# Optimization experiments

Measured on AMD Instinct MI355X. Metric: run time of the kernel, lower is better.

Reference implementation:

```python
import jax, jax.numpy as jnp
import numpy as np

B, T, D_MODEL, N_HEAD = 2, 2048, 1024, 16
HEAD_DIM = D_MODEL // N_HEAD


def setup_inputs() -> dict:
    key = jax.random.key(0)
    ks = jax.random.split(key, 4)
    s = 0.02
    return {
        "x": jax.random.normal(ks[0], (B, T, D_MODEL), dtype=jnp.float32),
        "freqs_cis": jnp.zeros((T, HEAD_DIM // 2), dtype=jnp.float32),  # unused under ALiBi
        "Wq": jax.random.normal(ks[1], (D_MODEL, D_MODEL), dtype=jnp.float32) * s,
        "bq": jnp.zeros((D_MODEL,), dtype=jnp.float32),
        "Wkv": jax.random.normal(ks[2], (2 * D_MODEL, D_MODEL), dtype=jnp.float32) * s,
        "bkv": jnp.zeros((2 * D_MODEL,), dtype=jnp.float32),
        "Wo": jax.random.normal(ks[3], (D_MODEL, D_MODEL), dtype=jnp.float32) * s,
        "bo": jnp.zeros((D_MODEL,), dtype=jnp.float32),
    }


def reference(x, freqs_cis, Wq, bq, Wkv, bkv, Wo, bo):
    Bb, Tt, C = x.shape
    H, Dh = N_HEAD, HEAD_DIM
    # projections (torch Linear: x @ W^T + b)
    q = (x @ Wq.T + bq).reshape(Bb, Tt, H, Dh).transpose(0, 2, 1, 3)      # [B,H,T,Dh]
    kv = (x @ Wkv.T + bkv).reshape(Bb, Tt, 2, H, Dh).transpose(2, 0, 3, 1, 4)
    k, v = kv[0], kv[1]                                                    # [B,H,T,Dh]
    scores = jnp.einsum('bhqd,bhkd->bhqk', q, k) * (1.0 / np.sqrt(Dh))
    # ALiBi: linear slopes (1/H ... 1.0), bias = slope * (j - i)
    slopes = jnp.arange(1, H + 1, dtype=jnp.float32) / H                   # [H]
    pos = jnp.arange(Tt, dtype=jnp.float32)
    dist = pos[None, :] - pos[:, None]                                     # [T,T], j - i
    scores = scores + slopes[:, None, None] * dist[None]                   # broadcast over B
    # causal mask (upper triangle -> -inf)
    causal = pos[:, None] >= pos[None, :]                                  # [T,T] keep-mask
    scores = jnp.where(causal[None, None], scores, -jnp.inf)
    attn = jax.nn.softmax(scores, axis=-1)
    y = jnp.einsum('bhqk,bhkd->bhqd', attn, v)                             # [B,H,T,Dh]
    y = y.transpose(0, 2, 1, 3).reshape(Bb, Tt, C)
    return y @ Wo.T + bo
```

## Files before the change

kernel.cpp:

```cpp
#include <hip/hip_runtime.h>

typedef unsigned short u16;
typedef __bf16 bf16x8 __attribute__((ext_vector_type(8)));
typedef unsigned short u16x8 __attribute__((ext_vector_type(8)));
typedef float f32x4 __attribute__((ext_vector_type(4)));

#define GP 72
#define KEY(r) ((((r) ^ ((r) >> 3)) & 7) << 3)
#define VKEY(d) ((((d) >> 3) & 7) << 3)

static __device__ __forceinline__ u16 f2b(float f) {
  union { float f; unsigned u; } x; x.f = f;
  unsigned r = x.u + 0x7FFFu + ((x.u >> 16) & 1u);
  return (u16)(r >> 16);
}

static __device__ __forceinline__ bf16x8 ld_frag(const u16* p) {
  union { u16x8 s; bf16x8 b; } u;
  u.s = *reinterpret_cast<const u16x8*>(p);
  return u.b;
}

__global__ __launch_bounds__(256) void cvt_f32_bf16(const float* __restrict__ in,
                                                    u16* __restrict__ out, int n4) {
  int i = blockIdx.x * 256 + threadIdx.x;
  if (i >= n4) return;
  float4 v = reinterpret_cast<const float4*>(in)[i];
  ushort4 o;
  o.x = f2b(v.x); o.y = f2b(v.y); o.z = f2b(v.z); o.w = f2b(v.w);
  reinterpret_cast<ushort4*>(out)[i] = o;
}

__global__ __launch_bounds__(256) void gemm_bt2(
    const u16* __restrict__ A, const u16* __restrict__ Bt,
    const float* __restrict__ bias, void* __restrict__ outp,
    int M, int N, int K, float scale, int out_bf16) {
  __shared__ alignas(16) u16 As[128 * 64];
  __shared__ alignas(16) u16 Bs[64 * 64];
  const int tid = threadIdx.x, wid = tid >> 6, lane = tid & 63;
  const int wr = wid >> 1, wc = wid & 1;
  const int row0 = blockIdx.x * 128, col0 = blockIdx.y * 64;
  const int lr = lane >> 3;
  const int lc = (lane & 7) * 8;
  const int frow = lane & 15, fk = (lane >> 4) * 8;
  f32x4 acc[4][2] = {};

  for (int k0 = 0; k0 < K; k0 += 64) {
    __syncthreads();
#pragma unroll
    for (int t = 0; t < 4; ++t) {
      const int r = wid * 32 + t * 8 + lr;
      __builtin_amdgcn_global_load_lds(
          (const __attribute__((address_space(1))) unsigned int*)(
              A + (size_t)(row0 + r) * K + k0 + (lc ^ KEY(r))),
          (__attribute__((address_space(3))) unsigned int*)(As + (wid * 32 + t * 8) * 64),
          16, 0, 0);
    }
#pragma unroll
    for (int t = 0; t < 2; ++t) {
      const int r = wid * 16 + t * 8 + lr;
      __builtin_amdgcn_global_load_lds(
          (const __attribute__((address_space(1))) unsigned int*)(
              Bt + (size_t)(col0 + r) * K + k0 + (lc ^ KEY(r))),
          (__attribute__((address_space(3))) unsigned int*)(Bs + (wid * 16 + t * 8) * 64),
          16, 0, 0);
    }
    __syncthreads();
#pragma unroll
    for (int ks = 0; ks < 2; ++ks) {
      bf16x8 a[4], b[2];
#pragma unroll
      for (int m = 0; m < 4; ++m) {
        const int r = wr * 64 + m * 16 + frow;
        a[m] = ld_frag(&As[r * 64 + ((ks * 32 + fk) ^ KEY(r))]);
      }
#pragma unroll
      for (int n = 0; n < 2; ++n) {
        const int r = wc * 32 + n * 16 + frow;
        b[n] = ld_frag(&Bs[r * 64 + ((ks * 32 + fk) ^ KEY(r))]);
      }
#pragma unroll
      for (int m = 0; m < 4; ++m)
#pragma unroll
        for (int n = 0; n < 2; ++n)
          acc[m][n] = __builtin_amdgcn_mfma_f32_16x16x32_bf16(a[m], b[n], acc[m][n], 0, 0, 0);
    }
  }
  const int colL = lane & 15, rb = (lane >> 4) * 4;
#pragma unroll
  for (int n = 0; n < 2; ++n) {
    const int gc = col0 + wc * 32 + n * 16 + colL;
    const float bv = bias[gc];
#pragma unroll
    for (int m = 0; m < 4; ++m)
#pragma unroll
      for (int r = 0; r < 4; ++r) {
        const int gr = row0 + wr * 64 + m * 16 + rb + r;
        const float v = (acc[m][n][r] + bv) * scale;
        if (out_bf16) reinterpret_cast<u16*>(outp)[(size_t)gr * N + gc] = f2b(v);
        else reinterpret_cast<float*>(outp)[(size_t)gr * N + gc] = v;
      }
  }
}

__global__ __launch_bounds__(256) void attn_kernel(
    const u16* __restrict__ qb,
    const u16* __restrict__ kvb,
    u16* __restrict__ yb,
    int T) {
  const int C = 1024;
  const int bh = blockIdx.x;
  const int qt = gridDim.y - 1 - blockIdx.y;
  const int b = bh >> 4, h = bh & 15;
  const float slope = (float)(h + 1) * 0.0625f;
  const int tid = threadIdx.x, wid = tid >> 6, lane = tid & 63;
  const int qBase = qt * 64;

  __shared__ alignas(16) u16 Ks[64 * GP];
  __shared__ alignas(16) u16 Vt[64 * GP];
  __shared__ alignas(16) u16 Ps[4][16 * GP];

  const int frow = lane & 15, fk = (lane >> 4) * 8;
  const int col = lane & 15, rb = (lane >> 4) * 4;

  const int q_row = qBase + wid * 16 + frow;
  const u16* qp = qb + (size_t)(b * T + q_row) * C + h * 64;
  const bf16x8 aq0 = ld_frag(qp + fk);
  const bf16x8 aq1 = ld_frag(qp + 32 + fk);

  float mrow[4] = {-1e30f, -1e30f, -1e30f, -1e30f};
  float lrow[4] = {0.f, 0.f, 0.f, 0.f};
  f32x4 accO[4] = {};

  const int sr = tid >> 3;
  const int sc = (tid & 7) * 8;

  for (int kt = 0; kt <= qt; ++kt) {
    const int kBase = kt * 64;
    __syncthreads();
    {
      const size_t g0 = (size_t)(b * T + kBase + sr) * 2048 + h * 64 + sc;
      const size_t g1 = (size_t)(b * T + kBase + sr + 32) * 2048 + h * 64 + sc;
      *reinterpret_cast<int4*>(&Ks[sr * GP + sc]) = *reinterpret_cast<const int4*>(&kvb[g0]);
      *reinterpret_cast<int4*>(&Ks[(sr + 32) * GP + sc]) = *reinterpret_cast<const int4*>(&kvb[g1]);
      int4 v0 = *reinterpret_cast<const int4*>(&kvb[g0 + 1024]);
      int4 v1 = *reinterpret_cast<const int4*>(&kvb[g1 + 1024]);
      const u16* p0 = reinterpret_cast<const u16*>(&v0);
      const u16* p1 = reinterpret_cast<const u16*>(&v1);
      const int kx = VKEY(sc);
#pragma unroll
      for (int j = 0; j < 8; ++j) {
        const int d = sc + j;
        Vt[d * GP + (sr ^ kx)] = p0[j];
        Vt[d * GP + ((sr + 32) ^ kx)] = p1[j];
      }
    }
    __syncthreads();

    f32x4 accS[4] = {};
#pragma unroll
    for (int n = 0; n < 4; ++n) {
      bf16x8 bk0 = ld_frag(&Ks[(n * 16 + frow) * GP + fk]);
      accS[n] = __builtin_amdgcn_mfma_f32_16x16x32_bf16(aq0, bk0, accS[n], 0, 0, 0);
      bf16x8 bk1 = ld_frag(&Ks[(n * 16 + frow) * GP + 32 + fk]);
      accS[n] = __builtin_amdgcn_mfma_f32_16x16x32_bf16(aq1, bk1, accS[n], 0, 0, 0);
    }

#pragma unroll
    for (int r = 0; r < 4; ++r) {
      const int qg = qBase + wid * 16 + rb + r;
      float s[4];
      float tmax = -1e30f;
#pragma unroll
      for (int n = 0; n < 4; ++n) {
        const int kg = kBase + n * 16 + col;
        float v = accS[n][r] + slope * (float)(kg - qg);
        if (kg > qg) v = -1e30f;
        s[n] = v;
        tmax = fmaxf(tmax, v);
      }
      tmax = fmaxf(tmax, __shfl_xor(tmax, 1));
      tmax = fmaxf(tmax, __shfl_xor(tmax, 2));
      tmax = fmaxf(tmax, __shfl_xor(tmax, 4));
      tmax = fmaxf(tmax, __shfl_xor(tmax, 8));
      const float newm = fmaxf(mrow[r], tmax);
      const float corr = __expf(mrow[r] - newm);
      mrow[r] = newm;
      float psum = 0.f;
#pragma unroll
      for (int n = 0; n < 4; ++n) {
        const float p = __expf(s[n] - newm);
        psum += p;
        Ps[wid][(rb + r) * GP + n * 16 + col] = f2b(p);
      }
      psum += __shfl_xor(psum, 1);
      psum += __shfl_xor(psum, 2);
      psum += __shfl_xor(psum, 4);
      psum += __shfl_xor(psum, 8);
      lrow[r] = lrow[r] * corr + psum;
#pragma unroll
      for (int n = 0; n < 4; ++n) accO[n][r] *= corr;
    }

#pragma unroll
    for (int ks = 0; ks < 2; ++ks) {
      bf16x8 ap = ld_frag(&Ps[wid][frow * GP + ks * 32 + fk]);
#pragma unroll
      for (int n = 0; n < 4; ++n) {
        const int d = n * 16 + frow;
        bf16x8 bv = ld_frag(&Vt[d * GP + ((ks * 32 + fk) ^ VKEY(d))]);
        accO[n] = __builtin_amdgcn_mfma_f32_16x16x32_bf16(ap, bv, accO[n], 0, 0, 0);
      }
    }
  }

#pragma unroll
  for (int r = 0; r < 4; ++r) {
    const float inv = 1.0f / lrow[r];
    const int qg = qBase + wid * 16 + rb + r;
    u16* yrow = yb + (size_t)(b * T + qg) * C + h * 64;
#pragma unroll
    for (int n = 0; n < 4; ++n) yrow[n * 16 + col] = f2b(accO[n][r] * inv);
  }
}

extern "C" void kernel_launch(void* const* d_in, const int* in_sizes, int n_in,
                              void* d_out, int out_size, void* d_ws, size_t ws_size,
                              hipStream_t stream) {
  const float* x   = (const float*)d_in[0];
  const float* Wq  = (const float*)d_in[2];
  const float* bq  = (const float*)d_in[3];
  const float* Wkv = (const float*)d_in[4];
  const float* bkv = (const float*)d_in[5];
  const float* Wo  = (const float*)d_in[6];
  const float* bo  = (const float*)d_in[7];
  float* out = (float*)d_out;

  const int B = 2, T = 2048, C = 1024;
  const int M = B * T;

  char* ws = (char*)d_ws;
  u16* xb   = (u16*)(ws + 0);
  u16* wqb  = (u16*)(ws + 8388608);
  u16* wkvb = (u16*)(ws + 10485760);
  u16* wob  = (u16*)(ws + 14680064);
  u16* qb   = (u16*)(ws + 16777216);
  u16* kvb  = (u16*)(ws + 25165824);
  u16* yb   = (u16*)(ws + 41943040);

  cvt_f32_bf16<<<(M * C / 4 + 255) / 256, 256, 0, stream>>>(x, xb, M * C / 4);
  cvt_f32_bf16<<<(C * C / 4 + 255) / 256, 256, 0, stream>>>(Wq, wqb, C * C / 4);
  cvt_f32_bf16<<<(2 * C * C / 4 + 255) / 256, 256, 0, stream>>>(Wkv, wkvb, 2 * C * C / 4);
  cvt_f32_bf16<<<(C * C / 4 + 255) / 256, 256, 0, stream>>>(Wo, wob, C * C / 4);

  gemm_bt2<<<dim3(M / 128, C / 64), 256, 0, stream>>>(xb, wqb, bq, qb, M, C, C, 0.125f, 1);
  gemm_bt2<<<dim3(M / 128, 2 * C / 64), 256, 0, stream>>>(xb, wkvb, bkv, kvb, M, 2 * C, C, 1.0f, 1);
  attn_kernel<<<dim3(B * 16, T / 64), 256, 0, stream>>>(qb, kvb, yb, T);
  gemm_bt2<<<dim3(M / 128, C / 64), 256, 0, stream>>>(yb, wob, bo, out, M, C, C, 1.0f, 0);
}
```

Before: 238.2 us.

## Fuse QKV GEMMs, enlarge GEMM tiles, restructure attention with prefetch and swizzle

Merges the Q and KV projection GEMMs into one launch and doubles the GEMM N-tile to 128, giving each block 4x4 MFMA accumulators for more operand reuse. The attention kernel now uses 32-query tiles with 2 waves per block and register-prefetches the next K/V tile while the current one is computed. It also replaces padded LDS rows with XOR swizzles, adds s_setprio around the MFMA sections, and hoists the ALiBi bias out of the row loop. The trade-offs are higher register pressure in the GEMM, fewer waves per attention block, and more attention blocks in total.

```diff
diff --git a/kernel.cpp b/kernel.cpp
--- a/kernel.cpp
+++ b/kernel.cpp
@@ -5,9 +5,7 @@
 typedef unsigned short u16x8 __attribute__((ext_vector_type(8)));
 typedef float f32x4 __attribute__((ext_vector_type(4)));
 
-#define GP 72
 #define KEY(r) ((((r) ^ ((r) >> 3)) & 7) << 3)
-#define VKEY(d) ((((d) >> 3) & 7) << 3)
 
 static __device__ __forceinline__ u16 f2b(float f) {
   union { float f; unsigned u; } x; x.f = f;
@@ -31,19 +29,19 @@
   reinterpret_cast<ushort4*>(out)[i] = o;
 }
 
-__global__ __launch_bounds__(256) void gemm_bt2(
+template <bool OUT_BF16>
+static __device__ __forceinline__ void gemm_body(
     const u16* __restrict__ A, const u16* __restrict__ Bt,
     const float* __restrict__ bias, void* __restrict__ outp,
-    int M, int N, int K, float scale, int out_bf16) {
+    int N, int K, int row0, int col0, float scale) {
   __shared__ alignas(16) u16 As[128 * 64];
-  __shared__ alignas(16) u16 Bs[64 * 64];
+  __shared__ alignas(16) u16 Bs[128 * 64];
   const int tid = threadIdx.x, wid = tid >> 6, lane = tid & 63;
   const int wr = wid >> 1, wc = wid & 1;
-  const int row0 = blockIdx.x * 128, col0 = blockIdx.y * 64;
   const int lr = lane >> 3;
   const int lc = (lane & 7) * 8;
   const int frow = lane & 15, fk = (lane >> 4) * 8;
-  f32x4 acc[4][2] = {};
+  f32x4 acc[4][4] = {};
 
   for (int k0 = 0; k0 < K; k0 += 64) {
     __syncthreads();
@@ -57,39 +55,39 @@
           16, 0, 0);
     }
 #pragma unroll
-    for (int t = 0; t < 2; ++t) {
-      const int r = wid * 16 + t * 8 + lr;
+    for (int t = 0; t < 4; ++t) {
+      const int r = wid * 32 + t * 8 + lr;
       __builtin_amdgcn_global_load_lds(
           (const __attribute__((address_space(1))) unsigned int*)(
               Bt + (size_t)(col0 + r) * K + k0 + (lc ^ KEY(r))),
-          (__attribute__((address_space(3))) unsigned int*)(Bs + (wid * 16 + t * 8) * 64),
+          (__attribute__((address_space(3))) unsigned int*)(Bs + (wid * 32 + t * 8) * 64),
           16, 0, 0);
     }
     __syncthreads();
 #pragma unroll
     for (int ks = 0; ks < 2; ++ks) {
-      bf16x8 a[4], b[2];
+      bf16x8 a[4], b[4];
 #pragma unroll
       for (int m = 0; m < 4; ++m) {
         const int r = wr * 64 + m * 16 + frow;
         a[m] = ld_frag(&As[r * 64 + ((ks * 32 + fk) ^ KEY(r))]);
       }
 #pragma unroll
-      for (int n = 0; n < 2; ++n) {
-        const int r = wc * 32 + n * 16 + frow;
+      for (int n = 0; n < 4; ++n) {
+        const int r = wc * 64 + n * 16 + frow;
         b[n] = ld_frag(&Bs[r * 64 + ((ks * 32 + fk) ^ KEY(r))]);
       }
 #pragma unroll
       for (int m = 0; m < 4; ++m)
 #pragma unroll
-        for (int n = 0; n < 2; ++n)
+        for (int n = 0; n < 4; ++n)
           acc[m][n] = __builtin_amdgcn_mfma_f32_16x16x32_bf16(a[m], b[n], acc[m][n], 0, 0, 0);
     }
   }
   const int colL = lane & 15, rb = (lane >> 4) * 4;
 #pragma unroll
-  for (int n = 0; n < 2; ++n) {
-    const int gc = col0 + wc * 32 + n * 16 + colL;
+  for (int n = 0; n < 4; ++n) {
+    const int gc = col0 + wc * 64 + n * 16 + colL;
     const float bv = bias[gc];
 #pragma unroll
     for (int m = 0; m < 4; ++m)
@@ -97,13 +95,33 @@
       for (int r = 0; r < 4; ++r) {
         const int gr = row0 + wr * 64 + m * 16 + rb + r;
         const float v = (acc[m][n][r] + bv) * scale;
-        if (out_bf16) reinterpret_cast<u16*>(outp)[(size_t)gr * N + gc] = f2b(v);
-        else reinterpret_cast<float*>(outp)[(size_t)gr * N + gc] = v;
-      }
-  }
-}
-
-__global__ __launch_bounds__(256) void attn_kernel(
+        if constexpr (OUT_BF16)
+          reinterpret_cast<u16*>(outp)[(size_t)gr * N + gc] = f2b(v);
+        else
+          reinterpret_cast<float*>(outp)[(size_t)gr * N + gc] = v;
+      }
+  }
+}
+
+__global__ __launch_bounds__(256) void gemm_qkv(
+    const u16* __restrict__ xb, const u16* __restrict__ wqb,
+    const u16* __restrict__ wkvb, const float* __restrict__ bq,
+    const float* __restrict__ bkv, u16* __restrict__ qb, u16* __restrict__ kvb) {
+  const int row0 = blockIdx.x * 128;
+  const int by = blockIdx.y;
+  const u16* Bt; const float* bias; u16* out; int N, col0; float scale;
+  if (by < 8) { Bt = wqb;  bias = bq;  out = qb;  N = 1024; col0 = by * 128;      scale = 0.125f; }
+  else        { Bt = wkvb; bias = bkv; out = kvb; N = 2048; col0 = (by - 8) * 128; scale = 1.0f; }
+  gemm_body<true>(xb, Bt, bias, out, N, 1024, row0, col0, scale);
+}
+
+__global__ __launch_bounds__(256) void gemm_o(
+    const u16* __restrict__ yb, const u16* __restrict__ wob,
+    const float* __restrict__ bo, float* __restrict__ out) {
+  gemm_body<false>(yb, wob, bo, out, 1024, 1024, blockIdx.x * 128, blockIdx.y * 128, 1.0f);
+}
+
+__global__ __launch_bounds__(128) void attn_kernel(
     const u16* __restrict__ qb,
     const u16* __restrict__ kvb,
     u16* __restrict__ yb,
@@ -114,14 +132,15 @@
   const int b = bh >> 4, h = bh & 15;
   const float slope = (float)(h + 1) * 0.0625f;
   const int tid = threadIdx.x, wid = tid >> 6, lane = tid & 63;
-  const int qBase = qt * 64;
-
-  __shared__ alignas(16) u16 Ks[64 * GP];
-  __shared__ alignas(16) u16 Vt[64 * GP];
-  __shared__ alignas(16) u16 Ps[4][16 * GP];
+  const int qBase = qt * 32;
+
+  __shared__ alignas(16) u16 Ks[64 * 64];
+  __shared__ alignas(16) u16 Vt[64 * 64];
+  __shared__ alignas(16) u16 Ps[2][16 * 64];
 
   const int frow = lane & 15, fk = (lane >> 4) * 8;
   const int col = lane & 15, rb = (lane >> 4) * 4;
+  const int pk = ((lane >> 4) & 3) << 3;
 
   const int q_row = qBase + wid * 16 + frow;
   const u16* qp = qb + (size_t)(b * T + q_row) * C + h * 64;
@@ -132,40 +151,60 @@
   float lrow[4] = {0.f, 0.f, 0.f, 0.f};
   f32x4 accO[4] = {};
 
-  const int sr = tid >> 3;
-  const int sc = (tid & 7) * 8;
-
-  for (int kt = 0; kt <= qt; ++kt) {
+  const int st_r = tid >> 3;
+  const int st_c = (tid & 7) * 8;
+  const int vkj = tid & 7;
+
+  const int nt = (qBase + 31) / 64 + 1;
+
+  int4 kreg[4], vreg[4];
+#pragma unroll
+  for (int t = 0; t < 4; ++t) {
+    const int r = st_r + 16 * t;
+    const size_t g = (size_t)(b * T + r) * 2048 + h * 64 + st_c;
+    kreg[t] = *reinterpret_cast<const int4*>(&kvb[g]);
+    vreg[t] = *reinterpret_cast<const int4*>(&kvb[g + 1024]);
+  }
+
+  for (int kt = 0; kt < nt; ++kt) {
     const int kBase = kt * 64;
+#pragma unroll
+    for (int t = 0; t < 4; ++t) {
+      const int r = st_r + 16 * t;
+      *reinterpret_cast<int4*>(&Ks[r * 64 + (st_c ^ KEY(r))]) = kreg[t];
+      const u16* pv = reinterpret_cast<const u16*>(&vreg[t]);
+#pragma unroll
+      for (int j = 0; j < 8; ++j) {
+        const int d = st_c + j;
+        Vt[d * 64 + (r ^ ((((j) ^ vkj) & 7) << 3))] = pv[j];
+      }
+    }
     __syncthreads();
-    {
-      const size_t g0 = (size_t)(b * T + kBase + sr) * 2048 + h * 64 + sc;
-      const size_t g1 = (size_t)(b * T + kBase + sr + 32) * 2048 + h * 64 + sc;
-      *reinterpret_cast<int4*>(&Ks[sr * GP + sc]) = *reinterpret_cast<const int4*>(&kvb[g0]);
-      *reinterpret_cast<int4*>(&Ks[(sr + 32) * GP + sc]) = *reinterpret_cast<const int4*>(&kvb[g1]);
-      int4 v0 = *reinterpret_cast<const int4*>(&kvb[g0 + 1024]);
-      int4 v1 = *reinterpret_cast<const int4*>(&kvb[g1 + 1024]);
-      const u16* p0 = reinterpret_cast<const u16*>(&v0);
-      const u16* p1 = reinterpret_cast<const u16*>(&v1);
-      const int kx = VKEY(sc);
-#pragma unroll
-      for (int j = 0; j < 8; ++j) {
-        const int d = sc + j;
-        Vt[d * GP + (sr ^ kx)] = p0[j];
-        Vt[d * GP + ((sr + 32) ^ kx)] = p1[j];
-      }
-    }
-    __syncthreads();
+    if (kt + 1 < nt) {
+#pragma unroll
+      for (int t = 0; t < 4; ++t) {
+        const int r = st_r + 16 * t;
+        const size_t g = (size_t)(b * T + kBase + 64 + r) * 2048 + h * 64 + st_c;
+        kreg[t] = *reinterpret_cast<const int4*>(&kvb[g]);
+        vreg[t] = *reinterpret_cast<const int4*>(&kvb[g + 1024]);
+      }
+    }
 
     f32x4 accS[4] = {};
+    __builtin_amdgcn_s_setprio(1);
 #pragma unroll
     for (int n = 0; n < 4; ++n) {
-      bf16x8 bk0 = ld_frag(&Ks[(n * 16 + frow) * GP + fk]);
+      const int r = n * 16 + frow;
+      bf16x8 bk0 = ld_frag(&Ks[r * 64 + (fk ^ KEY(r))]);
       accS[n] = __builtin_amdgcn_mfma_f32_16x16x32_bf16(aq0, bk0, accS[n], 0, 0, 0);
-      bf16x8 bk1 = ld_frag(&Ks[(n * 16 + frow) * GP + 32 + fk]);
+      bf16x8 bk1 = ld_frag(&Ks[r * 64 + ((32 + fk) ^ KEY(r))]);
       accS[n] = __builtin_amdgcn_mfma_f32_16x16x32_bf16(aq1, bk1, accS[n], 0, 0, 0);
     }
-
+    __builtin_amdgcn_s_setprio(0);
+
+    float bn[4]; int kg[4];
+#pragma unroll
+    for (int n = 0; n < 4; ++n) { kg[n] = kBase + n * 16 + col; bn[n] = slope * (float)kg[n]; }
 #pragma unroll
     for (int r = 0; r < 4; ++r) {
       const int qg = qBase + wid * 16 + rb + r;
@@ -173,9 +212,8 @@
       float tmax = -1e30f;
 #pragma unroll
       for (int n = 0; n < 4; ++n) {
-        const int kg = kBase + n * 16 + col;
-        float v = accS[n][r] + slope * (float)(kg - qg);
-        if (kg > qg) v = -1e30f;
+        float v = accS[n][r] + bn[n];
+        if (kg[n] > qg) v = -1e30f;
         s[n] = v;
         tmax = fmaxf(tmax, v);
       }
@@ -191,7 +229,7 @@
       for (int n = 0; n < 4; ++n) {
         const float p = __expf(s[n] - newm);
         psum += p;
-        Ps[wid][(rb + r) * GP + n * 16 + col] = f2b(p);
+        Ps[wid][(rb + r) * 64 + ((n * 16 + col) ^ pk)] = f2b(p);
       }
       psum += __shfl_xor(psum, 1);
       psum += __shfl_xor(psum, 2);
@@ -202,16 +240,20 @@
       for (int n = 0; n < 4; ++n) accO[n][r] *= corr;
     }
 
+    __builtin_amdgcn_s_setprio(1);
 #pragma unroll
     for (int ks = 0; ks < 2; ++ks) {
-      bf16x8 ap = ld_frag(&Ps[wid][frow * GP + ks * 32 + fk]);
+      const int pkr = ((frow >> 2) & 3) << 3;
+      bf16x8 ap = ld_frag(&Ps[wid][frow * 64 + ((ks * 32 + fk) ^ pkr)]);
 #pragma unroll
       for (int n = 0; n < 4; ++n) {
         const int d = n * 16 + frow;
-        bf16x8 bv = ld_frag(&Vt[d * GP + ((ks * 32 + fk) ^ VKEY(d))]);
+        bf16x8 bv = ld_frag(&Vt[d * 64 + ((ks * 32 + fk) ^ KEY(d))]);
         accO[n] = __builtin_amdgcn_mfma_f32_16x16x32_bf16(ap, bv, accO[n], 0, 0, 0);
       }
     }
+    __builtin_amdgcn_s_setprio(0);
+    __syncthreads();
   }
 
 #pragma unroll
@@ -253,8 +295,7 @@
   cvt_f32_bf16<<<(2 * C * C / 4 + 255) / 256, 256, 0, stream>>>(Wkv, wkvb, 2 * C * C / 4);
   cvt_f32_bf16<<<(C * C / 4 + 255) / 256, 256, 0, stream>>>(Wo, wob, C * C / 4);
 
-  gemm_bt2<<<dim3(M / 128, C / 64), 256, 0, stream>>>(xb, wqb, bq, qb, M, C, C, 0.125f, 1);
-  gemm_bt2<<<dim3(M / 128, 2 * C / 64), 256, 0, stream>>>(xb, wkvb, bkv, kvb, M, 2 * C, C, 1.0f, 1);
-  attn_kernel<<<dim3(B * 16, T / 64), 256, 0, stream>>>(qb, kvb, yb, T);
-  gemm_bt2<<<dim3(M / 128, C / 64), 256, 0, stream>>>(yb, wob, bo, out, M, C, C, 1.0f, 0);
-}
+  gemm_qkv<<<dim3(M / 128, 8 + 16), 256, 0, stream>>>(xb, wqb, wkvb, bq, bkv, qb, kvb);
+  attn_kernel<<<dim3(B * 16, T / 32), 128, 0, stream>>>(qb, kvb, yb, T);
+  gemm_o<<<dim3(M / 128, C / 128), 256, 0, stream>>>(yb, wob, bo, out);
+}
```

Result: slower. 259.4 us (+8.9%).
